# Performance work log

Hardware: AMD Instinct MI355X
Metric: run time of the kernel (lower is better)

The kernel has to match this reference:

```python
import jax, jax.numpy as jnp
import numpy as np

N_BLOCKS = 8
N_WIRES = 24
GAMMA, BETA, ALPHA = 0.1, 0.6, 0.15


def _apply_ry(state, w, theta):
    # RY(theta) = [[cos(t/2), -sin(t/2)], [sin(t/2), cos(t/2)]] on wire w.
    c = jnp.cos(theta * 0.5)
    s = jnp.sin(theta * 0.5)
    st = jnp.moveaxis(state, w, 0)  # (2, ...)
    new = jnp.stack([c * st[0] - s * st[1], s * st[0] + c * st[1]])
    return jnp.moveaxis(new, 0, w)


def _apply_cnot(state, ctrl, tgt):
    # Flip target bit where control bit == 1.
    st = jnp.moveaxis(state, (ctrl, tgt), (0, 1))  # (2, 2, ...)
    new = jnp.stack([st[0], st[1, ::-1]])
    return jnp.moveaxis(new, (0, 1), (ctrl, tgt))


def setup_inputs() -> dict:
    key = jax.random.key(0)
    angles = jax.random.normal(key, (N_BLOCKS, N_WIRES), dtype=jnp.float32)
    return {"angles": angles}


def reference(angles):
    n_blocks, n_wires = angles.shape  # static
    # Initial state |0...0>; RY and CNOT are real, so the state stays real.
    state = jnp.zeros((2,) * n_wires, dtype=angles.dtype).at[(0,) * n_wires].set(1.0)
    for k in range(n_blocks):
        for w in range(n_wires):
            state = _apply_ry(state, w, angles[k, w])
        for w in range(n_wires - 1):  # circular=False -> linear chain
            state = _apply_cnot(state, w, w + 1)
    probs = (state.reshape(-1) ** 2).reshape(2 ** n_wires, 1)  # |amp|^2
    easy_scale = 2.0 ** (n_wires - 1)
    x = (BETA * jnp.tanh(GAMMA * easy_scale * probs)) ** ALPHA
    return x - jnp.mean(x)
```

## Files before the change

### kernel.cpp

```cpp
#include <hip/hip_runtime.h>

#define NB 8
#define SSIZE (1u << 24)


__global__ void k_prep(const float* __restrict__ ang, double* __restrict__ dws) {
    int t = threadIdx.x;
    if (t == 0) dws[0] = 0.0;
    if (t < NB * 24) {
        double a = 0.5 * (double)ang[t];
        dws[8 + t]   = cos(a);
        dws[200 + t] = sin(a);
    }
}


__device__ __forceinline__ unsigned sw(unsigned f) {
    return f ^ (((f >> 3) ^ (f >> 5)) & 7u);
}

__device__ __forceinline__ void ry2d(double& a0, double& a1, double c, double s, bool ctl) {
    double w0 = c * a0 - s * a1;
    double w1 = s * a0 + c * a1;
    a0 = ctl ? w1 : w0;
    a1 = ctl ? w0 : w1;
}

template<int TB, int MODE>
__device__ __forceinline__ void stage8d(double4* x, double c, double s) {
#pragma unroll
    for (int j0 = 0; j0 < 8; ++j0) {
        if (j0 & (1 << TB)) continue;
        const int j1 = j0 | (1 << TB);
        const bool ctl = (MODE == 1) || (MODE == 0 && ((j0 >> (TB + 1)) & 1));
        ry2d(x[j0].x, x[j1].x, c, s, ctl);
        ry2d(x[j0].y, x[j1].y, c, s, ctl);
        ry2d(x[j0].z, x[j1].z, c, s, ctl);
        ry2d(x[j0].w, x[j1].w, c, s, ctl);
    }
}

__device__ __forceinline__ void coefs_d(unsigned lane, int lb, bool g,
                                        double c, double s, double& cA, double& cP) {
    bool b = (lane >> lb) & 1u;
    cA = g ? (b ? -s : s) : c;
    cP = g ? c : (b ? s : -s);
}


template<int CTRL>
__device__ __forceinline__ double dpp_xor_d(double v) {
    int lo = __builtin_amdgcn_mov_dpp(__double2loint(v), CTRL, 0xf, 0xf, true);
    int hi = __builtin_amdgcn_mov_dpp(__double2hiint(v), CTRL, 0xf, 0xf, true);
    return __hiloint2double(hi, lo);
}

template<int CTRL>
__device__ __forceinline__ void lane_stage_dpp(double4* x, double cA, double cP) {
#pragma unroll
    for (int j = 0; j < 8; ++j) {
        double px = dpp_xor_d<CTRL>(x[j].x);
        double py = dpp_xor_d<CTRL>(x[j].y);
        double pz = dpp_xor_d<CTRL>(x[j].z);
        double pw = dpp_xor_d<CTRL>(x[j].w);
        x[j].x = cA * x[j].x + cP * px;
        x[j].y = cA * x[j].y + cP * py;
        x[j].z = cA * x[j].z + cP * pz;
        x[j].w = cA * x[j].w + cP * pw;
    }
}

__device__ __forceinline__ void lane_stage_sw4(double4* x, double cA, double cP) {
#pragma unroll
    for (int j = 0; j < 8; ++j) {
        double px = __shfl_xor(x[j].x, 4, 64);
        double py = __shfl_xor(x[j].y, 4, 64);
        double pz = __shfl_xor(x[j].z, 4, 64);
        double pw = __shfl_xor(x[j].w, 4, 64);
        x[j].x = cA * x[j].x + cP * px;
        x[j].y = cA * x[j].y + cP * py;
        x[j].z = cA * x[j].z + cP * pz;
        x[j].w = cA * x[j].w + cP * pw;
    }
}

template<bool IS32>
__device__ __forceinline__ void swap_pair_d(double& a, double& b) {
    int alo = __double2loint(a), ahi = __double2hiint(a);
    int blo = __double2loint(b), bhi = __double2hiint(b);
    if (IS32) {
        auto r0 = __builtin_amdgcn_permlane32_swap(alo, blo, false, false);
        auto r1 = __builtin_amdgcn_permlane32_swap(ahi, bhi, false, false);
        alo = r0[0]; blo = r0[1]; ahi = r1[0]; bhi = r1[1];
    } else {
        auto r0 = __builtin_amdgcn_permlane16_swap(alo, blo, false, false);
        auto r1 = __builtin_amdgcn_permlane16_swap(ahi, bhi, false, false);
        alo = r0[0]; blo = r0[1]; ahi = r1[0]; bhi = r1[1];
    }
    a = __hiloint2double(ahi, alo);
    b = __hiloint2double(bhi, blo);
}

template<bool IS32>
__device__ __forceinline__ void stage_swap(double4* x, double c, double s, bool gsel) {
    double al = gsel ? s : c, be = gsel ? c : -s;
    double ga = gsel ? c : s, de = gsel ? -s : c;
#pragma unroll
    for (int p = 0; p < 4; ++p) {
        double4& A = x[2 * p];
        double4& B = x[2 * p + 1];
        swap_pair_d<IS32>(A.x, B.x); swap_pair_d<IS32>(A.y, B.y);
        swap_pair_d<IS32>(A.z, B.z); swap_pair_d<IS32>(A.w, B.w);
        double ux = A.x, vx = B.x, uy = A.y, vy = B.y;
        double uz = A.z, vz = B.z, uw = A.w, vw = B.w;
        A.x = al * ux + be * vx;  B.x = ga * ux + de * vx;
        A.y = al * uy + be * vy;  B.y = ga * uy + de * vy;
        A.z = al * uz + be * vz;  B.z = ga * uz + de * vz;
        A.w = al * uw + be * vw;  B.w = ga * uw + de * vw;
        swap_pair_d<IS32>(A.x, B.x); swap_pair_d<IS32>(A.y, B.y);
        swap_pair_d<IS32>(A.z, B.z); swap_pair_d<IS32>(A.w, B.w);
    }
}

__device__ __forceinline__ void dstages_d(double4* x, double c1, double s1, bool g1,
                                          double c0, double s0) {
#pragma unroll
    for (int j = 0; j < 8; ++j) {
        ry2d(x[j].x, x[j].z, c1, s1, g1);
        ry2d(x[j].y, x[j].w, c1, s1, g1);
        ry2d(x[j].x, x[j].y, c0, s0, false);
        ry2d(x[j].z, x[j].w, c0, s0, true);
    }
}

__device__ __forceinline__ float xform(float z) {
    float e2 = __builtin_amdgcn_exp2f(z * 2.8853900817779268f);
    float big = 1.0f - 2.0f * __builtin_amdgcn_rcpf(e2 + 1.0f);
    float z2 = z * z;
    float small_ = z * (1.0f - 0.33333333f * z2 * (1.0f - 0.4f * z2));
    float t = (z < 0.04f) ? small_ : big;
    return __builtin_amdgcn_exp2f(0.15f * __builtin_amdgcn_logf(0.6f * t));
}


__device__ __forceinline__ float4 lo4(const double4 v) {
    return make_float4(__int_as_float(__double2loint(v.x)),
                       __int_as_float(__double2loint(v.y)),
                       __int_as_float(__double2loint(v.z)),
                       __int_as_float(__double2loint(v.w)));
}
__device__ __forceinline__ float4 hi4(const double4 v) {
    return make_float4(__int_as_float(__double2hiint(v.x)),
                       __int_as_float(__double2hiint(v.y)),
                       __int_as_float(__double2hiint(v.z)),
                       __int_as_float(__double2hiint(v.w)));
}
__device__ __forceinline__ double4 mk4(const float4 h, const float4 l) {
    return make_double4(__hiloint2double(__float_as_int(h.x), __float_as_int(l.x)),
                        __hiloint2double(__float_as_int(h.y), __float_as_int(l.y)),
                        __hiloint2double(__float_as_int(h.z), __float_as_int(l.z)),
                        __hiloint2double(__float_as_int(h.w), __float_as_int(l.w)));
}

__device__ __forceinline__ void t_fwd_d(float4* T4, double4* x, unsigned tid,
                                        unsigned lane, unsigned hi, bool protect) {
    if (protect) __syncthreads();
#pragma unroll
    for (int jj = 0; jj < 8; ++jj) T4[sw(tid | (jj << 9))] = lo4(x[jj]);
    __syncthreads();
    float4 tl[8];
#pragma unroll
    for (int jj = 0; jj < 8; ++jj) tl[jj] = T4[sw(lane | (jj << 6) | hi)];
    __syncthreads();
#pragma unroll
    for (int jj = 0; jj < 8; ++jj) T4[sw(tid | (jj << 9))] = hi4(x[jj]);
    __syncthreads();
#pragma unroll
    for (int jj = 0; jj < 8; ++jj)
        x[jj] = mk4(T4[sw(lane | (jj << 6) | hi)], tl[jj]);
}

__device__ __forceinline__ void t_back_d(float4* T4, double4* x, unsigned tid,
                                         unsigned lane, unsigned hi) {
    __syncthreads();
#pragma unroll
    for (int jj = 0; jj < 8; ++jj) T4[sw(lane | (jj << 6) | hi)] = lo4(x[jj]);
    __syncthreads();
    float4 tl[8];
#pragma unroll
    for (int jj = 0; jj < 8; ++jj) tl[jj] = T4[sw(tid | (jj << 9))];
    __syncthreads();
#pragma unroll
    for (int jj = 0; jj < 8; ++jj) T4[sw(lane | (jj << 6) | hi)] = hi4(x[jj]);
    __syncthreads();
#pragma unroll
    for (int jj = 0; jj < 8; ++jj)
        x[jj] = mk4(T4[sw(tid | (jj << 9))], tl[jj]);
}

template<int START>
__device__ __forceinline__ void jj_trio_d(double4* x, const double* c, const double* s,
                                          bool top_on) {
    if (START == 0) {
        if (top_on) stage8d<2, 1>(x, c[0], s[0]);
        else        stage8d<2,-1>(x, c[0], s[0]);
    }
    if (START <= 1) stage8d<1, 0>(x, c[1], s[1]);
    stage8d<0, 0>(x, c[2], s[2]);
}

template<int N>
__device__ __forceinline__ void lane_ladder_v(double4* x, unsigned lane,
                                              const double* c, const double* s) {
    const bool hi5 = lane >= 32;
    stage_swap<true>(x, c[0], s[0], hi5);
    if (N > 1) stage_swap<false>(x, c[1], s[1], hi5);
    if (N > 2) { double cA, cP; coefs_d(lane, 3, (lane >> 4) & 1, c[2], s[2], cA, cP);
                 lane_stage_dpp<0x128>(x, cA, cP); }
    if (N > 3) { double cA, cP; coefs_d(lane, 2, (lane >> 3) & 1, c[3], s[3], cA, cP);
                 lane_stage_sw4(x, cA, cP); }
    if (N > 4) { double cA, cP; coefs_d(lane, 1, (lane >> 2) & 1, c[4], s[4], cA, cP);
                 lane_stage_dpp<0x4E>(x, cA, cP); }
    if (N > 5) { double cA, cP; coefs_d(lane, 0, (lane >> 1) & 1, c[5], s[5], cA, cP);
                 lane_stage_dpp<0xB1>(x, cA, cP); }
}

__device__ __forceinline__ double4 d4_of(const float4 f) {
    return make_double4((double)f.x, (double)f.y, (double)f.z, (double)f.w);
}
__device__ __forceinline__ float4 f4_of(const double4 d) {
    return make_float4((float)d.x, (float)d.y, (float)d.z, (float)d.w);
}

template<int I, int NBLK>
__device__ __forceinline__ void h_block(double4* x, float4* T4,
                                        const double* __restrict__ dws, int kbase,
                                        unsigned tid, unsigned lane, unsigned hi) {
    const double* C = dws + 8   + (kbase + I) * 24;
    const double* S = dws + 200 + (kbase + I) * 24;
    jj_trio_d<0>(x, C + 0, S + 0, false);
    t_fwd_d(T4, x, tid, lane, hi, I > 0);
    jj_trio_d<0>(x, C + 3, S + 3, (tid & 64u) != 0);
    lane_ladder_v<6 - I>(x, lane, C + 6, S + 6);
    if constexpr (I < NBLK - 1) {
        t_back_d(T4, x, tid, lane, hi);
        h_block<I + 1, NBLK>(x, T4, dws, kbase, tid, lane, hi);
    }
}

template<int NBLK, int INIT>
__global__ __launch_bounds__(512, 2) void k_H(float* __restrict__ st,
                                              const double* __restrict__ dws,
                                              int kbase) {
    __shared__ float4 T4[4096];
    const unsigned bid = blockIdx.x;
    const unsigned m = (bid >> 3) | ((bid & 7u) << 7);
    const unsigned tid = threadIdx.x;
    const unsigned lane = tid & 63u;
    const unsigned hi = (tid >> 6) << 9;
    float4* G4 = reinterpret_cast<float4*>(st);
    double4 x[8];

    if (INIT) {
        const double* C0 = dws + 8;
        const double* S0 = dws + 200;
        double P = 1.0;
#pragma unroll
        for (int b = 2; b <= 10; ++b) {
            unsigned g = ((m >> (b - 2)) ^ (m >> (b - 1))) & 1u;
            P *= g ? S0[23 - b] : C0[23 - b];
        }
        { unsigned g = ((m >> 9) ^ tid) & 1u; P *= g ? S0[12] : C0[12]; }
#pragma unroll
        for (int b = 12; b <= 19; ++b) {
            unsigned g = ((tid >> (b - 12)) ^ (tid >> (b - 11))) & 1u;
            P *= g ? S0[23 - b] : C0[23 - b];
        }
        double D[4];
#pragma unroll
        for (int d = 0; d < 4; ++d) {
            unsigned g0 = (d ^ (d >> 1)) & 1u;
            unsigned g1 = ((d >> 1) ^ m) & 1u;
            D[d] = (g0 ? S0[23] : C0[23]) * (g1 ? S0[22] : C0[22]);
        }
        unsigned t8 = (tid >> 8) & 1u;
#pragma unroll
        for (int jj = 0; jj < 8; ++jj) {
            unsigned g20 = (t8 ^ (unsigned)jj) & 1u;
            unsigned g21 = ((unsigned)jj ^ ((unsigned)jj >> 1)) & 1u;
            unsigned g22 = (((unsigned)jj >> 1) ^ ((unsigned)jj >> 2)) & 1u;
            unsigned g23 = (((unsigned)jj >> 2)) & 1u;
            double J = (g20 ? S0[3] : C0[3]) * (g21 ? S0[2] : C0[2]) *
                       (g22 ? S0[1] : C0[1]) * (g23 ? S0[0] : C0[0]);
            double PJ = P * J;
            x[jj] = make_double4(PJ * D[0], PJ * D[1], PJ * D[2], PJ * D[3]);
        }
    } else {
#pragma unroll
        for (int jj = 0; jj < 8; ++jj) {
            unsigned w = tid | (jj << 9);
            x[jj] = d4_of(G4[m | (w << 10)]);
        }
    }

    h_block<0, NBLK>(x, T4, dws, kbase, tid, lane, hi);

#pragma unroll
    for (int jj = 0; jj < 8; ++jj) {
        unsigned w = lane | (jj << 6) | hi;
        G4[m | (w << 10)] = f4_of(x[jj]);
    }
}

template<int NBLK, int FUSE>
__global__ __launch_bounds__(512, 2) void k_L(float* __restrict__ st,
                                              double* __restrict__ dws,
                                              int kbase) {
    __shared__ float4 T4[4096];
    const unsigned m = blockIdx.x;
    const unsigned tid = threadIdx.x;
    const unsigned lane = tid & 63u;
    const unsigned hi = (tid >> 6) << 9;
    float4* G4 = reinterpret_cast<float4*>(st) + (m << 12);
    double4 x[8];
#pragma unroll
    for (int jj = 0; jj < 8; ++jj) x[jj] = d4_of(G4[tid + (jj << 9)]);

#pragma unroll
    for (int i = 0; i < NBLK; ++i) {
        const double* C = dws + 8   + (kbase + i) * 24;
        const double* S = dws + 200 + (kbase + i) * 24;
        if (i == 0)      jj_trio_d<2>(x, C + 10, S + 10, false);
        else if (i == 1) jj_trio_d<1>(x, C + 10, S + 10, false);
        else             jj_trio_d<0>(x, C + 10, S + 10, (m & 1u) != 0);
        t_fwd_d(T4, x, tid, lane, hi, i > 0);
        jj_trio_d<0>(x, C + 13, S + 13, (tid & 64u) != 0);
        lane_ladder_v<6>(x, lane, C + 16, S + 16);
        dstages_d(x, C[22], S[22], lane & 1u, C[23], S[23]);
        if (i < NBLK - 1) t_back_d(T4, x, tid, lane, hi);
    }

    if (FUSE) {
        double lsum = 0.0;
#pragma unroll
        for (int jj = 0; jj < 8; ++jj) {
            double* v = &x[jj].x;
            float4 o;
            float* ov = &o.x;
#pragma unroll
            for (int d = 0; d < 4; ++d) {
                float z = (float)(838860.8 * v[d] * v[d]);
                float xf = xform(z);
                ov[d] = xf;
                lsum += (double)xf;
            }
            G4[lane | (jj << 6) | hi] = o;
        }
#pragma unroll
        for (int o = 32; o > 0; o >>= 1) lsum += __shfl_down(lsum, o, 64);
        __syncthreads();
        double* wsum = reinterpret_cast<double*>(T4);
        if ((tid & 63u) == 0) wsum[tid >> 6] = lsum;
        __syncthreads();
        if (tid == 0) {
            double b = 0.0;
#pragma unroll
            for (int i = 0; i < 8; ++i) b += wsum[i];
            atomicAdd(dws, b);
        }
    } else {
#pragma unroll
        for (int jj = 0; jj < 8; ++jj) G4[lane | (jj << 6) | hi] = f4_of(x[jj]);
    }
}

__global__ void k_final(float* __restrict__ st, const double* __restrict__ dws) {
    unsigned idx = blockIdx.x * blockDim.x + threadIdx.x;
    unsigned stride = gridDim.x * blockDim.x;
    float mean = (float)(dws[0] * (1.0 / 16777216.0));
    float4* G4 = reinterpret_cast<float4*>(st);
    for (unsigned q = idx; q < (SSIZE / 4); q += stride) {
        float4 v = G4[q];
        v.x -= mean; v.y -= mean; v.z -= mean; v.w -= mean;
        G4[q] = v;
    }
}

extern "C" void kernel_launch(void* const* d_in, const int* in_sizes, int n_in,
                              void* d_out, int out_size, void* d_ws, size_t ws_size,
                              hipStream_t stream) {
    const float* ang = (const float*)d_in[0];
    float* st = (float*)d_out;
    double* dws = (double*)d_ws;

    k_prep<<<1, 256, 0, stream>>>(ang, dws);
    k_H<3, 1><<<1024, 512, 0, stream>>>(st, dws, 1);
    k_L<3, 0><<<1024, 512, 0, stream>>>(st, dws, 1);
    k_H<3, 0><<<1024, 512, 0, stream>>>(st, dws, 4);
    k_L<3, 0><<<1024, 512, 0, stream>>>(st, dws, 4);
    k_H<1, 0><<<1024, 512, 0, stream>>>(st, dws, 7);
    k_L<1, 1><<<1024, 512, 0, stream>>>(st, dws, 7);
    k_final<<<4096, 256, 0, stream>>>(st, dws);
}
```

Measured before the change: 575.3 us.

## Reorganize wire-to-lane mapping in L kernel and stage final output via LDS

Changes the global layout of the state so the H kernel reads and writes groups of four contiguous float4s instead of single float4s strided by 1024, which should improve coalescing. The L kernel's gate sequence is rewritten to match: some wires move onto lanes via DPP and swizzle stages, and a new runtime-controlled stage8d_rt variant is added. The fused final pass now transposes its output through shared memory so global stores are contiguous. This adds extra LDS traffic and barriers and relies on the new bit mapping being consistent across both kernels.

```diff
diff --git a/kernel.cpp b/kernel.cpp
--- a/kernel.cpp
+++ b/kernel.cpp
@@ -33,6 +33,19 @@
         if (j0 & (1 << TB)) continue;
         const int j1 = j0 | (1 << TB);
         const bool ctl = (MODE == 1) || (MODE == 0 && ((j0 >> (TB + 1)) & 1));
+        ry2d(x[j0].x, x[j1].x, c, s, ctl);
+        ry2d(x[j0].y, x[j1].y, c, s, ctl);
+        ry2d(x[j0].z, x[j1].z, c, s, ctl);
+        ry2d(x[j0].w, x[j1].w, c, s, ctl);
+    }
+}
+
+template<int TB>
+__device__ __forceinline__ void stage8d_rt(double4* x, double c, double s, bool ctl) {
+#pragma unroll
+    for (int j0 = 0; j0 < 8; ++j0) {
+        if (j0 & (1 << TB)) continue;
+        const int j1 = j0 | (1 << TB);
         ry2d(x[j0].x, x[j1].x, c, s, ctl);
         ry2d(x[j0].y, x[j1].y, c, s, ctl);
         ry2d(x[j0].z, x[j1].z, c, s, ctl);
@@ -258,6 +271,7 @@
     const unsigned tid = threadIdx.x;
     const unsigned lane = tid & 63u;
     const unsigned hi = (tid >> 6) << 9;
+    const unsigned mbase4 = ((m & 3u) << 2) | ((m >> 2) << 4);
     float4* G4 = reinterpret_cast<float4*>(st);
     double4 x[8];
 
@@ -299,7 +313,7 @@
 #pragma unroll
         for (int jj = 0; jj < 8; ++jj) {
             unsigned w = tid | (jj << 9);
-            x[jj] = d4_of(G4[m | (w << 10)]);
+            x[jj] = d4_of(G4[mbase4 | (w & 3u) | ((w >> 2) << 12)]);
         }
     }
 
@@ -308,7 +322,7 @@
 #pragma unroll
     for (int jj = 0; jj < 8; ++jj) {
         unsigned w = lane | (jj << 6) | hi;
-        G4[m | (w << 10)] = f4_of(x[jj]);
+        G4[mbase4 | (w & 3u) | ((w >> 2) << 12)] = f4_of(x[jj]);
     }
 }
 
@@ -330,18 +344,36 @@
     for (int i = 0; i < NBLK; ++i) {
         const double* C = dws + 8   + (kbase + i) * 24;
         const double* S = dws + 200 + (kbase + i) * 24;
-        if (i == 0)      jj_trio_d<2>(x, C + 10, S + 10, false);
-        else if (i == 1) jj_trio_d<1>(x, C + 10, S + 10, false);
-        else             jj_trio_d<0>(x, C + 10, S + 10, (m & 1u) != 0);
+        if (i >= 2) {
+            double cA, cP; coefs_d(lane, 1, (m & 1u) != 0, C[10], S[10], cA, cP);
+            lane_stage_dpp<0x4E>(x, cA, cP);
+        }
+        if (i >= 1) {
+            double cA, cP; coefs_d(lane, 0, (lane >> 1) & 1, C[11], S[11], cA, cP);
+            lane_stage_dpp<0xB1>(x, cA, cP);
+        }
+        stage8d_rt<2>(x, C[12], S[12], (lane & 1u) != 0);
+        stage8d<1, 0>(x, C[13], S[13]);
+        stage8d<0, 0>(x, C[14], S[14]);
         t_fwd_d(T4, x, tid, lane, hi, i > 0);
-        jj_trio_d<0>(x, C + 13, S + 13, (tid & 64u) != 0);
-        lane_ladder_v<6>(x, lane, C + 16, S + 16);
-        dstages_d(x, C[22], S[22], lane & 1u, C[23], S[23]);
+        if (tid & 64u) stage8d<2, 1>(x, C[15], S[15]);
+        else           stage8d<2,-1>(x, C[15], S[15]);
+        stage8d<1, 0>(x, C[16], S[16]);
+        stage8d<0, 0>(x, C[17], S[17]);
+        stage_swap<true >(x, C[18], S[18], lane >= 32);
+        stage_swap<false>(x, C[19], S[19], lane >= 32);
+        { double cA, cP; coefs_d(lane, 3, (lane >> 4) & 1, C[20], S[20], cA, cP);
+          lane_stage_dpp<0x128>(x, cA, cP); }
+        { double cA, cP; coefs_d(lane, 2, (lane >> 3) & 1, C[21], S[21], cA, cP);
+          lane_stage_sw4(x, cA, cP); }
+        dstages_d(x, C[22], S[22], ((lane >> 2) & 1u) != 0,
+                  C[23], S[23]);
         if (i < NBLK - 1) t_back_d(T4, x, tid, lane, hi);
     }
 
     if (FUSE) {
         double lsum = 0.0;
+        __syncthreads();
 #pragma unroll
         for (int jj = 0; jj < 8; ++jj) {
             double* v = &x[jj].x;
@@ -354,8 +386,14 @@
                 ov[d] = xf;
                 lsum += (double)xf;
             }
-            G4[lane | (jj << 6) | hi] = o;
-        }
+            unsigned t4 = ((lane >> 2) & 0xFu) | ((unsigned)jj << 4)
+                        | (((tid >> 6) & 7u) << 7) | ((lane & 3u) << 10);
+            T4[sw(t4)] = o;
+        }
+        __syncthreads();
+#pragma unroll
+        for (int jj = 0; jj < 8; ++jj)
+            G4[tid | (jj << 9)] = T4[sw(tid | (jj << 9))];
 #pragma unroll
         for (int o = 32; o > 0; o >>= 1) lsum += __shfl_down(lsum, o, 64);
         __syncthreads();
@@ -370,7 +408,8 @@
         }
     } else {
 #pragma unroll
-        for (int jj = 0; jj < 8; ++jj) G4[lane | (jj << 6) | hi] = f4_of(x[jj]);
+        for (int jj = 0; jj < 8; ++jj)
+            G4[lane | (jj << 6) | hi] = f4_of(x[jj]);
     }
 }
 
```

After: 561.4 us. 1.02x faster.
